# Kernel tuning notes

Hardware: AMD Instinct MI355X
Metric: run time of the kernel (lower is better)

The kernel has to match this reference:

```python
import jax, jax.numpy as jnp
import numpy as np

B, S = 8, 2048
CLIP, H, BN, NC = 512, 512, 256, 10
LN_EPS = 1e-5


def _ln(x, g, b):
    mu = x.mean(-1, keepdims=True)
    var = ((x - mu) ** 2).mean(-1, keepdims=True)
    return (x - mu) * jax.lax.rsqrt(var + LN_EPS) * g + b


def setup_inputs() -> dict:
    key = jax.random.key(0)
    ks = jax.random.split(key, 16)
    sc = lambda i, shp: jax.random.normal(ks[i], shp, jnp.float32) * 0.02
    inp = {
        "local_feat": jax.random.normal(ks[0], (B, S, CLIP), jnp.float32),
        "coords": jax.random.uniform(ks[1], (B, S, 3), jnp.float32),
        "mask": jax.random.randint(ks[2], (B, S), 0, 2) > 0,
        # node encoder
        "w_enc": sc(3, (CLIP, H)), "b_enc": jnp.zeros((H,), jnp.float32),
        "ln1_g": jnp.ones((H,), jnp.float32), "ln1_b": jnp.zeros((H,), jnp.float32),
        # attention projections
        "wq": sc(4, (H, H)), "bq": jnp.zeros((H,), jnp.float32),
        "wk": sc(5, (H, H)), "bk": jnp.zeros((H,), jnp.float32),
        "wv": sc(6, (H, H)), "bv": jnp.zeros((H,), jnp.float32),
        # bottleneck
        "w_bn": sc(7, (H, BN)), "b_bn": jnp.zeros((BN,), jnp.float32),
        "ln2_g": jnp.ones((BN,), jnp.float32), "ln2_b": jnp.zeros((BN,), jnp.float32),
        # classifier
        "w_c1": sc(8, (BN, BN // 2)), "b_c1": jnp.zeros((BN // 2,), jnp.float32),
        "w_c2": sc(9, (BN // 2, NC)), "b_c2": jnp.zeros((NC,), jnp.float32),
    }
    return inp


def reference(local_feat, coords, mask, w_enc, b_enc, ln1_g, ln1_b,
              wq, bq, wk, bk, wv, bv, w_bn, b_bn, ln2_g, ln2_b,
              w_c1, b_c1, w_c2, b_c2):
    # node encoder (dropout is identity in eval)
    h = jax.nn.relu(_ln(local_feat @ w_enc + b_enc, ln1_g, ln1_b))  # [B,S,H]

    # pairwise euclidean distance on (x,y), exp-modulated adjacency
    pos = coords[:, :, :2]
    diff = pos[:, :, None, :] - pos[:, None, :, :]              # [B,S,S,2]
    sq = jnp.sum(diff * diff, axis=-1)                          # [B,S,S]
    dist = jnp.sqrt(jnp.where(sq > 0, sq, 1.0))
    dist = jnp.where(sq > 0, dist, 0.0)
    spatial_adj = jnp.exp(-dist * 5.0)

    q = h @ wq + bq
    k = h @ wk + bk
    v = h @ wv + bv
    scores = jnp.einsum("bsd,btd->bst", q, k) / jnp.sqrt(jnp.float32(H))
    attn = jax.nn.softmax(scores, axis=-1) * spatial_adj        # [B,S,S]
    attn = jnp.where(mask[:, None, :], 0.0, attn)               # zero padded keys

    h_graph = jnp.einsum("bst,btd->bsd", attn, v)               # [B,S,H]
    out = jax.nn.relu(_ln(h_graph @ w_bn + b_bn, ln2_g, ln2_b)) # [B,S,BN]

    valid = (~mask)[:, :, None].astype(out.dtype)               # [B,S,1]
    pooled = (out * valid).sum(1) / jnp.clip(valid.sum(1), 1e-9, None)

    logits = jax.nn.relu(pooled @ w_c1 + b_c1) @ w_c2 + b_c2    # [B,NC]
    return logits, pooled
```

## Files before the change

### kernel.cpp

```cpp
#include <hip/hip_runtime.h>
#include <hip/hip_bf16.h>
#include <stdint.h>


typedef __hip_bfloat16 bf16_t;
typedef __attribute__((ext_vector_type(8))) short bf16x8;
typedef __attribute__((ext_vector_type(4))) float f32x4;

__device__ __forceinline__ void cp16_to_lds(const void* g, void* lds) {
  __builtin_amdgcn_global_load_lds(
      (__attribute__((address_space(1))) void*)(g),
      (__attribute__((address_space(3))) void*)(lds), 16, 0, 0);
}

__device__ __forceinline__ uint pk2(float a, float b) {
  bf16_t x = __float2bfloat16(a), y = __float2bfloat16(b);
  return ((uint)(*(ushort*)&y) << 16) | (*(ushort*)&x);
}
__device__ __forceinline__ float bflo(uint u) { return __uint_as_float(u << 16); }
__device__ __forceinline__ float bfhi(uint u) { return __uint_as_float(u & 0xffff0000u); }

__global__ __launch_bounds__(256) void gemm_bt(
    const bf16_t* __restrict__ A, const bf16_t* __restrict__ B,
    void* __restrict__ Cv, const float* __restrict__ bias, int biasStride,
    float scale, int K, long sA, long sB, long sC, int ldC, int mode)
{
  __shared__ __align__(16) char smem[32768];
  bf16_t* lA = (bf16_t*)smem;
  bf16_t* lB = (bf16_t*)(smem + 16384);
  const int z = blockIdx.z;
  A += (long)z * sA;
  B += (long)z * sB;
  const float* bz = bias ? bias + (long)z * biasStride : nullptr;
  const int m0 = blockIdx.y * 128, n0 = blockIdx.x * 128;
  const int tid = threadIdx.x;
  const int w = tid >> 6, lane = tid & 63;
  const int wm = w >> 1, wn = w & 1;

  const int rr = tid >> 2;
  const int cc = (((tid & 3) ^ ((tid >> 3) & 3)) * 8);
  const bf16_t* a0 = A + (long)(m0 + rr) * K + cc;
  const bf16_t* b0 = B + (long)(n0 + rr) * K + cc;
  const long rowskip = (long)64 * K;

  char* lAc = (char*)lA;
  char* lBc = (char*)lB;
  const int ofs0 = w * 1024;
  const int ofs1 = 4096 + w * 1024;

  f32x4 acc[4][4] = {};
  const int nkt = K >> 6;
  const int quad = lane >> 4;
  const int rsel = lane & 15;
  const int swz = (rsel >> 1) & 3;
  const int kchunkA = (quad ^ swz) * 8;

  for (int kt = 0; kt < nkt; ++kt) {
    __syncthreads();
    cp16_to_lds(a0,                 lAc + ofs0);
    cp16_to_lds(a0 + rowskip,       lAc + ofs1);
    cp16_to_lds(a0 + 32,            lAc + 8192 + ofs0);
    cp16_to_lds(a0 + 32 + rowskip,  lAc + 8192 + ofs1);
    cp16_to_lds(b0,                 lBc + ofs0);
    cp16_to_lds(b0 + rowskip,       lBc + ofs1);
    cp16_to_lds(b0 + 32,            lBc + 8192 + ofs0);
    cp16_to_lds(b0 + 32 + rowskip,  lBc + 8192 + ofs1);
    a0 += 64; b0 += 64;
    __syncthreads();

#pragma unroll
    for (int p = 0; p < 2; ++p) {
      const int pb = p * 4096;
      bf16x8 af[4], bfr[4];
#pragma unroll
      for (int i = 0; i < 4; ++i) {
        af[i]  = *(const bf16x8*)&lA[pb + (wm * 64 + i * 16 + rsel) * 32 + kchunkA];
        bfr[i] = *(const bf16x8*)&lB[pb + (wn * 64 + i * 16 + rsel) * 32 + kchunkA];
      }
#pragma unroll
      for (int i = 0; i < 4; ++i)
#pragma unroll
        for (int j = 0; j < 4; ++j)
          acc[i][j] = __builtin_amdgcn_mfma_f32_16x16x32_bf16(af[i], bfr[j], acc[i][j], 0, 0, 0);
    }
  }

  const int col = lane & 15;
  float bv4[4];
#pragma unroll
  for (int j = 0; j < 4; ++j) {
    const int ng = n0 + wn * 64 + j * 16 + col;
    bv4[j] = bz ? bz[ng] : 0.0f;
  }

  if (mode == 0) {
    char* stb = smem + w * 2176;
    const int nc0 = n0 + wn * 64;
#pragma unroll
    for (int i = 0; i < 4; ++i) {
      __syncthreads();
      bf16_t* st = (bf16_t*)stb;
#pragma unroll
      for (int j = 0; j < 4; ++j)
#pragma unroll
        for (int r = 0; r < 4; ++r)
          st[(quad * 4 + r) * 68 + j * 16 + col] =
              __float2bfloat16(acc[i][j][r] * scale + bv4[j]);
      __syncthreads();
      const int row16 = lane >> 2, cseg = lane & 3;
      const long mrow = m0 + wm * 64 + i * 16 + row16;
      bf16_t* cp = (bf16_t*)Cv + (long)z * sC + mrow * ldC + nc0 + cseg * 16;
      const char* sp = stb + row16 * 136 + cseg * 32;
#pragma unroll
      for (int hh = 0; hh < 2; ++hh) {
        uint2 aa = *(const uint2*)(sp + hh * 16);
        uint2 bb = *(const uint2*)(sp + hh * 16 + 8);
        uint4 vv; vv.x = aa.x; vv.y = aa.y; vv.z = bb.x; vv.w = bb.y;
        *(uint4*)(cp + hh * 8) = vv;
      }
    }
  } else {
#pragma unroll
    for (int j = 0; j < 4; ++j) {
      const int ng = n0 + wn * 64 + j * 16 + col;
#pragma unroll
      for (int i = 0; i < 4; ++i) {
        const int mg = m0 + wm * 64 + i * 16 + quad * 4;
#pragma unroll
        for (int r = 0; r < 4; ++r)
          ((float*)Cv)[(long)z * sC + (long)(mg + r) * ldC + ng] =
              acc[i][j][r] * scale + bv4[j];
      }
    }
  }
}

__global__ __launch_bounds__(256) void weight_prep(
    const float* __restrict__ w0, const float* __restrict__ w1,
    const float* __restrict__ w2, const float* __restrict__ w3,
    const float* __restrict__ w4,
    const float* __restrict__ bq, const float* __restrict__ bk,
    const float* __restrict__ bv,
    bf16_t* __restrict__ outT, float* __restrict__ bias_cat)
{
  const int z = blockIdx.z;
  const int N = (z == 4) ? 256 : 512;
  if (z == 4 && blockIdx.y >= 4) return;
  const float* in = (z == 0) ? w0 : (z == 1) ? w1 : (z == 2) ? w2 : (z == 3) ? w3 : w4;
  bf16_t* out = outT + (long)z * 262144;
  const int k0 = blockIdx.x * 64, n0 = blockIdx.y * 64;
  __shared__ bf16_t tile[64 * 66];
  const int tid = threadIdx.x;
  const int r = tid >> 2, c4 = tid & 3;
  const float* src = in + (long)(k0 + r) * N + n0 + c4 * 16;
  uint* dst = (uint*)&tile[r * 66 + c4 * 16];
  float4 f0 = ((const float4*)src)[0], f1 = ((const float4*)src)[1];
  float4 f2 = ((const float4*)src)[2], f3 = ((const float4*)src)[3];
  dst[0] = pk2(f0.x, f0.y); dst[1] = pk2(f0.z, f0.w);
  dst[2] = pk2(f1.x, f1.y); dst[3] = pk2(f1.z, f1.w);
  dst[4] = pk2(f2.x, f2.y); dst[5] = pk2(f2.z, f2.w);
  dst[6] = pk2(f3.x, f3.y); dst[7] = pk2(f3.z, f3.w);
  __syncthreads();
  bf16_t* og = out + (long)(n0 + r) * 512 + k0 + c4 * 16;
  uint ov[8];
#pragma unroll
  for (int j = 0; j < 16; j += 2) {
    const ushort lo = *(const ushort*)&tile[(c4 * 16 + j) * 66 + r];
    const ushort hi = *(const ushort*)&tile[(c4 * 16 + j + 1) * 66 + r];
    ov[j >> 1] = ((uint)hi << 16) | lo;
  }
  uint4 o0, o1;
  o0.x = ov[0]; o0.y = ov[1]; o0.z = ov[2]; o0.w = ov[3];
  o1.x = ov[4]; o1.y = ov[5]; o1.z = ov[6]; o1.w = ov[7];
  ((uint4*)og)[0] = o0;
  ((uint4*)og)[1] = o1;
  if (z >= 1 && z <= 3 && blockIdx.x == 0 && blockIdx.y == 0) {
    const float* bs = (z == 1) ? bq : (z == 2) ? bk : bv;
    bias_cat[(z - 1) * 512 + tid] = bs[tid];
    bias_cat[(z - 1) * 512 + 256 + tid] = bs[256 + tid];
  }
}

__global__ __launch_bounds__(256) void transpose_bf16_k(
    const bf16_t* __restrict__ in, bf16_t* __restrict__ o)
{
  __shared__ bf16_t tile[64 * 66];
  const int b = blockIdx.z, t0 = blockIdx.x * 64, d0 = blockIdx.y * 64;
  const int tid = threadIdx.x;
  const int r = tid >> 2, c4 = tid & 3;
  const uint4* src = (const uint4*)(in + ((long)b * 2048 + t0 + r) * 512 + d0 + c4 * 16);
  uint* dst = (uint*)&tile[r * 66 + c4 * 16];
  uint4 g0 = src[0], g1 = src[1];
  dst[0] = g0.x; dst[1] = g0.y; dst[2] = g0.z; dst[3] = g0.w;
  dst[4] = g1.x; dst[5] = g1.y; dst[6] = g1.z; dst[7] = g1.w;
  __syncthreads();
  bf16_t* dstg = o + ((long)b * 512 + d0 + r) * 2048 + t0 + c4 * 16;
  uint ov[8];
#pragma unroll
  for (int k = 0; k < 16; k += 2) {
    const ushort lo = *(const ushort*)&tile[(c4 * 16 + k) * 66 + r];
    const ushort hi = *(const ushort*)&tile[(c4 * 16 + k + 1) * 66 + r];
    ov[k >> 1] = ((uint)hi << 16) | lo;
  }
  uint4 o0, o1;
  o0.x = ov[0]; o0.y = ov[1]; o0.z = ov[2]; o0.w = ov[3];
  o1.x = ov[4]; o1.y = ov[5]; o1.z = ov[6]; o1.w = ov[7];
  ((uint4*)dstg)[0] = o0;
  ((uint4*)dstg)[1] = o1;
}

__global__ __launch_bounds__(256) void cast_bf16_v(
    const float4* __restrict__ in, uint2* __restrict__ o, int n4) {
  const int i = blockIdx.x * 256 + threadIdx.x;
  if (i < n4) {
    const float4 f = in[i];
    uint2 r; r.x = pk2(f.x, f.y); r.y = pk2(f.z, f.w);
    o[i] = r;
  }
}

__global__ __launch_bounds__(256) void ln_relu_h(
    bf16_t* __restrict__ X, const float* __restrict__ g, const float* __restrict__ b)
{
  const int tid = threadIdx.x;
  const int lane = tid & 63, w = tid >> 6;
  const long row = (long)blockIdx.x * 4 + w;
  bf16_t* xp = X + row * 512 + lane * 8;
  const uint4 pkv = *(const uint4*)xp;
  const uint va[4] = {pkv.x, pkv.y, pkv.z, pkv.w};
  float v[8];
  float s = 0.0f, q = 0.0f;
#pragma unroll
  for (int i = 0; i < 4; ++i) {
    v[2 * i] = bflo(va[i]); v[2 * i + 1] = bfhi(va[i]);
    s += v[2 * i] + v[2 * i + 1];
    q += v[2 * i] * v[2 * i] + v[2 * i + 1] * v[2 * i + 1];
  }
  for (int o = 32; o; o >>= 1) { s += __shfl_down(s, o); q += __shfl_down(q, o); }
  s = __shfl(s, 0); q = __shfl(q, 0);
  const float mu = s * (1.0f / 512.0f);
  const float rs = rsqrtf(q * (1.0f / 512.0f) - mu * mu + 1e-5f);
  const float4 g0 = ((const float4*)(g + lane * 8))[0], g1 = ((const float4*)(g + lane * 8))[1];
  const float4 b0 = ((const float4*)(b + lane * 8))[0], b1 = ((const float4*)(b + lane * 8))[1];
  const float gg[8] = {g0.x, g0.y, g0.z, g0.w, g1.x, g1.y, g1.z, g1.w};
  const float bb[8] = {b0.x, b0.y, b0.z, b0.w, b1.x, b1.y, b1.z, b1.w};
  uint ov[4];
#pragma unroll
  for (int i = 0; i < 4; ++i) {
    const float y0 = fmaxf((v[2 * i] - mu) * rs * gg[2 * i] + bb[2 * i], 0.0f);
    const float y1 = fmaxf((v[2 * i + 1] - mu) * rs * gg[2 * i + 1] + bb[2 * i + 1], 0.0f);
    ov[i] = pk2(y0, y1);
  }
  uint4 st; st.x = ov[0]; st.y = ov[1]; st.z = ov[2]; st.w = ov[3];
  *(uint4*)xp = st;
}

__global__ __launch_bounds__(256) void softmax_adj(
    bf16_t* __restrict__ SC, const float* __restrict__ coords,
    const int* __restrict__ mask)
{
  const int bs = blockIdx.x;
  const int b = bs >> 11, s = bs & 2047;
  const long base = (long)bs * 2048;
  const int tid = threadIdx.x;
  const uint4 pkv = *(const uint4*)(SC + base + tid * 8);
  const uint va[4] = {pkv.x, pkv.y, pkv.z, pkv.w};
  float rv[8];
  float mx = -3.0e38f;
#pragma unroll
  for (int i = 0; i < 4; ++i) {
    rv[2 * i] = bflo(va[i]); rv[2 * i + 1] = bfhi(va[i]);
    mx = fmaxf(mx, fmaxf(rv[2 * i], rv[2 * i + 1]));
  }
  for (int o = 32; o; o >>= 1) mx = fmaxf(mx, __shfl_down(mx, o));
  __shared__ float sm[8];
  const int w = tid >> 6, lane = tid & 63;
  if (!lane) sm[w] = mx;
  __syncthreads();
  mx = fmaxf(fmaxf(sm[0], sm[1]), fmaxf(sm[2], sm[3]));
  float sum = 0.0f;
#pragma unroll
  for (int i = 0; i < 8; ++i) { rv[i] = __expf(rv[i] - mx); sum += rv[i]; }
  for (int o = 32; o; o >>= 1) sum += __shfl_down(sum, o);
  if (!lane) sm[4 + w] = sum;
  __syncthreads();
  const float inv = 1.0f / (sm[4] + sm[5] + sm[6] + sm[7]);
  const float px = coords[((long)b * 2048 + s) * 3];
  const float py = coords[((long)b * 2048 + s) * 3 + 1];
  const int t0 = tid * 8;
  const float* cb = coords + ((long)b * 2048 + t0) * 3;
  const int* mb = mask + b * 2048 + t0;
  uint ov[4];
#pragma unroll
  for (int i = 0; i < 8; ++i) {
    const float dx = px - cb[i * 3], dy = py - cb[i * 3 + 1];
    const float adj = __expf(-5.0f * sqrtf(dx * dx + dy * dy));
    const float val = mb[i] ? 0.0f : rv[i] * inv * adj;
    bf16_t bt = __float2bfloat16(val);
    const ushort u = *(const ushort*)&bt;
    if (i & 1) ov[i >> 1] |= ((uint)u << 16);
    else       ov[i >> 1] = u;
  }
  uint4 st; st.x = ov[0]; st.y = ov[1]; st.z = ov[2]; st.w = ov[3];
  *(uint4*)(SC + base + t0) = st;
}

__global__ __launch_bounds__(256) void ln2_pool(
    const float* __restrict__ X, const float* __restrict__ g, const float* __restrict__ bt,
    const int* __restrict__ mask, float* __restrict__ pacc)
{
  const int tid = threadIdx.x;
  const int row0 = blockIdx.x * 16;
  const int w = tid >> 6, lane = tid & 63;
  __shared__ float sm[8];
  const float gv = g[tid], bv = bt[tid];
  float acc = 0.0f;
  for (int r = 0; r < 16; ++r) {
    const int row = row0 + r;
    const float x = X[(long)row * 256 + tid];
    float s = x, q = x * x;
    for (int o = 32; o; o >>= 1) { s += __shfl_down(s, o); q += __shfl_down(q, o); }
    if (!lane) { sm[w] = s; sm[4 + w] = q; }
    __syncthreads();
    const float S = sm[0] + sm[1] + sm[2] + sm[3];
    const float Q = sm[4] + sm[5] + sm[6] + sm[7];
    const float mu = S * (1.0f / 256.0f);
    const float rs = rsqrtf(Q * (1.0f / 256.0f) - mu * mu + 1e-5f);
    const float y = fmaxf((x - mu) * rs * gv + bv, 0.0f);
    if (!mask[row]) acc += y;
    __syncthreads();
  }
  atomicAdd(&pacc[(row0 >> 11) * 256 + tid], acc);
}

__global__ __launch_bounds__(256) void classifier_k(
    const float* __restrict__ pacc, const int* __restrict__ mask,
    const float* __restrict__ w1, const float* __restrict__ b1,
    const float* __restrict__ w2, const float* __restrict__ b2,
    float* __restrict__ out)
{
  const int tid = threadIdx.x;
  __shared__ float pooled[2048];
  __shared__ float hidden[1024];
  __shared__ float cnt[8];
  if (tid < 8) cnt[tid] = 0.0f;
  __syncthreads();
  {
    const int* mb = mask + tid * 64;
    int c = 0;
#pragma unroll 8
    for (int i = 0; i < 64; ++i) c += mb[i] ? 0 : 1;
    atomicAdd(&cnt[tid >> 5], (float)c);
  }
  __syncthreads();
  for (int i = tid; i < 2048; i += 256) {
    const float p = pacc[i] / fmaxf(cnt[i >> 8], 1e-9f);
    pooled[i] = p;
    out[80 + i] = p;
  }
  __syncthreads();
  for (int o = tid; o < 1024; o += 256) {
    const int bb = o >> 7, j = o & 127;
    float s = b1[j];
    const float* pb = pooled + bb * 256;
    for (int c = 0; c < 256; ++c) s += pb[c] * w1[c * 128 + j];
    hidden[o] = fmaxf(s, 0.0f);
  }
  __syncthreads();
  if (tid < 80) {
    const int bb = tid / 10, j = tid - bb * 10;
    float s = b2[j];
    const float* hb = hidden + bb * 128;
    for (int c = 0; c < 128; ++c) s += hb[c] * w2[c * 10 + j];
    out[tid] = s;
  }
}

extern "C" void kernel_launch(void* const* d_in, const int* in_sizes, int n_in,
                              void* d_out, int out_size, void* d_ws, size_t ws_size,
                              hipStream_t stream)
{
  const float* lf   = (const float*)d_in[0];
  const float* co   = (const float*)d_in[1];
  const int*   mk   = (const int*)d_in[2];
  const float* wenc = (const float*)d_in[3];
  const float* benc = (const float*)d_in[4];
  const float* g1   = (const float*)d_in[5];
  const float* be1  = (const float*)d_in[6];
  const float* wq   = (const float*)d_in[7];
  const float* bq   = (const float*)d_in[8];
  const float* wk   = (const float*)d_in[9];
  const float* bk   = (const float*)d_in[10];
  const float* wv   = (const float*)d_in[11];
  const float* bvp  = (const float*)d_in[12];
  const float* wbn  = (const float*)d_in[13];
  const float* bbn  = (const float*)d_in[14];
  const float* g2   = (const float*)d_in[15];
  const float* be2  = (const float*)d_in[16];
  const float* w1   = (const float*)d_in[17];
  const float* b1   = (const float*)d_in[18];
  const float* w2   = (const float*)d_in[19];
  const float* b2   = (const float*)d_in[20];
  float* out = (float*)d_out;
  char* ws = (char*)d_ws;

  bf16_t* featb = (bf16_t*)(ws + 0);
  bf16_t* wT    = (bf16_t*)(ws + 16777216);
  bf16_t* wencT = wT;
  bf16_t* wqT   = wT + 262144;
  bf16_t* wbnT  = wT + 4 * 262144;
  float*  bias_cat = (float*)(ws + 19398656);
  bf16_t* h     = (bf16_t*)(ws + 19404800);
  bf16_t* qkv   = (bf16_t*)(ws + 36182016);
  bf16_t* vT    = (bf16_t*)(ws + 86513664);
  bf16_t* sc    = (bf16_t*)(ws + 103290880);
  bf16_t* hg    = (bf16_t*)(ws + 0);
  float*  bnp   = (float*)(ws + 36182016);
  float*  pacc  = (float*)(ws + 52959232);

  if (ws_size < 170399744) return;

  cast_bf16_v<<<8192, 256, 0, stream>>>((const float4*)lf, (uint2*)featb, 2097152);
  weight_prep<<<dim3(8, 8, 5), 256, 0, stream>>>(wenc, wq, wk, wv, wbn, bq, bk, bvp,
                                                 wT, bias_cat);

  gemm_bt<<<dim3(4, 128, 1), 256, 0, stream>>>(featb, wencT, h, benc, 0, 1.0f, 512,
                                               0, 0, 0, 512, 0);
  ln_relu_h<<<4096, 256, 0, stream>>>(h, g1, be1);
  gemm_bt<<<dim3(4, 128, 3), 256, 0, stream>>>(h, wqT, qkv, bias_cat, 512, 1.0f, 512,
                                               0, 262144, 8388608, 512, 0);
  transpose_bf16_k<<<dim3(32, 8, 8), 256, 0, stream>>>(qkv + 16777216, vT);
  gemm_bt<<<dim3(16, 16, 8), 256, 0, stream>>>(qkv, qkv + 8388608, sc, nullptr, 0,
                                               0.044194173824159216f, 512,
                                               1048576, 1048576, 4194304, 2048, 0);
  softmax_adj<<<16384, 256, 0, stream>>>(sc, co, mk);
  gemm_bt<<<dim3(4, 16, 8), 256, 0, stream>>>(sc, vT, hg, nullptr, 0, 1.0f, 2048,
                                              4194304, 1048576, 1048576, 512, 0);
  gemm_bt<<<dim3(2, 128, 1), 256, 0, stream>>>(hg, wbnT, bnp, bbn, 0, 1.0f, 512,
                                               0, 0, 0, 256, 2);
  hipMemsetAsync(pacc, 0, 8192, stream);
  ln2_pool<<<1024, 256, 0, stream>>>(bnp, g2, be2, mk, pacc);
  classifier_k<<<1, 256, 0, stream>>>(pacc, mk, w1, b1, w2, b2, out);
}
```

Baseline: 405.7 us.

## Double-buffer GEMM K-panels to overlap global-to-LDS loads with MFMA

Restructures the gemm_bt main loop into 32-wide K panels held in two LDS buffers. The next panel is issued with global_load_lds while MFMAs run on the current one, so load latency is hidden behind compute rather than exposed between barriers. Barrier count per 64 of K stays the same. The scheme relies on the barrier waiting for the outstanding async LDS loads, and it only speeds up the GEMM parts of the pipeline.

```diff
diff --git a/kernel.cpp b/kernel.cpp
--- a/kernel.cpp
+++ b/kernel.cpp
@@ -49,41 +49,44 @@
   const int ofs1 = 4096 + w * 1024;
 
   f32x4 acc[4][4] = {};
-  const int nkt = K >> 6;
   const int quad = lane >> 4;
   const int rsel = lane & 15;
   const int swz = (rsel >> 1) & 3;
   const int kchunkA = (quad ^ swz) * 8;
 
-  for (int kt = 0; kt < nkt; ++kt) {
+#define STAGE(kofs, bofs) do {                                   \
+    cp16_to_lds(a0 + (kofs),           lAc + (bofs) + ofs0);     \
+    cp16_to_lds(a0 + (kofs) + rowskip, lAc + (bofs) + ofs1);     \
+    cp16_to_lds(b0 + (kofs),           lBc + (bofs) + ofs0);     \
+    cp16_to_lds(b0 + (kofs) + rowskip, lBc + (bofs) + ofs1);     \
+  } while (0)
+
+#define COMPUTE(pbase) do {                                                        \
+    bf16x8 af[4], bfr[4];                                                          \
+    _Pragma("unroll")                                                              \
+    for (int i = 0; i < 4; ++i) {                                                  \
+      af[i]  = *(const bf16x8*)&lA[(pbase) + (wm * 64 + i * 16 + rsel) * 32 + kchunkA]; \
+      bfr[i] = *(const bf16x8*)&lB[(pbase) + (wn * 64 + i * 16 + rsel) * 32 + kchunkA]; \
+    }                                                                              \
+    _Pragma("unroll")                                                              \
+    for (int i = 0; i < 4; ++i)                                                    \
+      _Pragma("unroll")                                                            \
+      for (int j = 0; j < 4; ++j)                                                  \
+        acc[i][j] = __builtin_amdgcn_mfma_f32_16x16x32_bf16(af[i], bfr[j], acc[i][j], 0, 0, 0); \
+  } while (0)
+
+  const int npan = K >> 5;
+  STAGE(0, 0);
+  for (int pp = 0; pp < npan; pp += 2) {
     __syncthreads();
-    cp16_to_lds(a0,                 lAc + ofs0);
-    cp16_to_lds(a0 + rowskip,       lAc + ofs1);
-    cp16_to_lds(a0 + 32,            lAc + 8192 + ofs0);
-    cp16_to_lds(a0 + 32 + rowskip,  lAc + 8192 + ofs1);
-    cp16_to_lds(b0,                 lBc + ofs0);
-    cp16_to_lds(b0 + rowskip,       lBc + ofs1);
-    cp16_to_lds(b0 + 32,            lBc + 8192 + ofs0);
-    cp16_to_lds(b0 + 32 + rowskip,  lBc + 8192 + ofs1);
-    a0 += 64; b0 += 64;
+    STAGE((pp + 1) * 32, 8192);
+    COMPUTE(0);
     __syncthreads();
-
-#pragma unroll
-    for (int p = 0; p < 2; ++p) {
-      const int pb = p * 4096;
-      bf16x8 af[4], bfr[4];
-#pragma unroll
-      for (int i = 0; i < 4; ++i) {
-        af[i]  = *(const bf16x8*)&lA[pb + (wm * 64 + i * 16 + rsel) * 32 + kchunkA];
-        bfr[i] = *(const bf16x8*)&lB[pb + (wn * 64 + i * 16 + rsel) * 32 + kchunkA];
-      }
-#pragma unroll
-      for (int i = 0; i < 4; ++i)
-#pragma unroll
-        for (int j = 0; j < 4; ++j)
-          acc[i][j] = __builtin_amdgcn_mfma_f32_16x16x32_bf16(af[i], bfr[j], acc[i][j], 0, 0, 0);
-    }
-  }
+    if (pp + 2 < npan) STAGE((pp + 2) * 32, 0);
+    COMPUTE(4096);
+  }
+#undef STAGE
+#undef COMPUTE
 
   const int col = lane & 15;
   float bv4[4];
```

Result: slower. 414.7 us (+2.2%).

## Emit Q/K as fp8 and V transposed from QKV GEMM; fp8 score GEMM

Applied to the files above, without the earlier changes.

The QKV projection becomes a dedicated kernel that writes Q and K as fp8 bytes and writes V directly in transposed bf16 layout, so the separate transpose kernel is no longer needed. The score GEMM now reads fp8 Q/K and uses fp8 MFMA instructions, which halves its operand bytes and doubles the k-depth per load. This lowers memory traffic and removes one launch. The cost is reduced precision in the attention scores, which could hurt accuracy.

```diff
diff --git a/kernel.cpp b/kernel.cpp
--- a/kernel.cpp
+++ b/kernel.cpp
@@ -4,6 +4,7 @@
 
 
 typedef __hip_bfloat16 bf16_t;
+typedef unsigned char u8;
 typedef __attribute__((ext_vector_type(8))) short bf16x8;
 typedef __attribute__((ext_vector_type(4))) float f32x4;
 
@@ -131,6 +132,218 @@
           ((float*)Cv)[(long)z * sC + (long)(mg + r) * ldC + ng] =
               acc[i][j][r] * scale + bv4[j];
       }
+    }
+  }
+}
+
+__global__ __launch_bounds__(256) void gemm_qkv(
+    const bf16_t* __restrict__ A, const bf16_t* __restrict__ wT,
+    const float* __restrict__ bias_cat, u8* __restrict__ o8,
+    bf16_t* __restrict__ vT)
+{
+  __shared__ __align__(16) char smem[32768];
+  bf16_t* lA = (bf16_t*)smem;
+  bf16_t* lB = (bf16_t*)(smem + 16384);
+  const int z = blockIdx.z;
+  const bf16_t* B = wT + (long)(z + 1) * 262144;
+  const float* bz = bias_cat + (long)z * 512;
+  const int K = 512;
+  const int m0 = blockIdx.y * 128, n0 = blockIdx.x * 128;
+  const int tid = threadIdx.x;
+  const int w = tid >> 6, lane = tid & 63;
+  const int wm = w >> 1, wn = w & 1;
+
+  const int rr = tid >> 2;
+  const int cc = (((tid & 3) ^ ((tid >> 3) & 3)) * 8);
+  const bf16_t* a0 = A + (long)(m0 + rr) * K + cc;
+  const bf16_t* b0 = B + (long)(n0 + rr) * K + cc;
+  const long rowskip = (long)64 * K;
+
+  char* lAc = (char*)lA;
+  char* lBc = (char*)lB;
+  const int ofs0 = w * 1024;
+  const int ofs1 = 4096 + w * 1024;
+
+  f32x4 acc[4][4] = {};
+  const int quad = lane >> 4;
+  const int rsel = lane & 15;
+  const int swz = (rsel >> 1) & 3;
+  const int kchunkA = (quad ^ swz) * 8;
+
+  for (int kt = 0; kt < 8; ++kt) {
+    __syncthreads();
+    cp16_to_lds(a0,                 lAc + ofs0);
+    cp16_to_lds(a0 + rowskip,       lAc + ofs1);
+    cp16_to_lds(a0 + 32,            lAc + 8192 + ofs0);
+    cp16_to_lds(a0 + 32 + rowskip,  lAc + 8192 + ofs1);
+    cp16_to_lds(b0,                 lBc + ofs0);
+    cp16_to_lds(b0 + rowskip,       lBc + ofs1);
+    cp16_to_lds(b0 + 32,            lBc + 8192 + ofs0);
+    cp16_to_lds(b0 + 32 + rowskip,  lBc + 8192 + ofs1);
+    a0 += 64; b0 += 64;
+    __syncthreads();
+
+#pragma unroll
+    for (int p = 0; p < 2; ++p) {
+      const int pb = p * 4096;
+      bf16x8 af[4], bfr[4];
+#pragma unroll
+      for (int i = 0; i < 4; ++i) {
+        af[i]  = *(const bf16x8*)&lA[pb + (wm * 64 + i * 16 + rsel) * 32 + kchunkA];
+        bfr[i] = *(const bf16x8*)&lB[pb + (wn * 64 + i * 16 + rsel) * 32 + kchunkA];
+      }
+#pragma unroll
+      for (int i = 0; i < 4; ++i)
+#pragma unroll
+        for (int j = 0; j < 4; ++j)
+          acc[i][j] = __builtin_amdgcn_mfma_f32_16x16x32_bf16(af[i], bfr[j], acc[i][j], 0, 0, 0);
+    }
+  }
+
+  const int col = lane & 15;
+  float bv4[4];
+#pragma unroll
+  for (int j = 0; j < 4; ++j) bv4[j] = bz[n0 + wn * 64 + j * 16 + col];
+  const int nc0 = n0 + wn * 64;
+
+  if (z < 2) {
+    u8* stb = (u8*)(smem + w * 2176);
+    u8* O = o8 + (long)z * 8388608;
+#pragma unroll
+    for (int i = 0; i < 4; ++i) {
+      __syncthreads();
+#pragma unroll
+      for (int j = 0; j < 4; ++j) {
+        uint pk = 0;
+        pk = __builtin_amdgcn_cvt_pk_fp8_f32(acc[i][j][0] + bv4[j],
+                                             acc[i][j][1] + bv4[j], pk, false);
+        pk = __builtin_amdgcn_cvt_pk_fp8_f32(acc[i][j][2] + bv4[j],
+                                             acc[i][j][3] + bv4[j], pk, true);
+        stb[(quad * 4 + 0) * 72 + j * 16 + col] = (u8)(pk);
+        stb[(quad * 4 + 1) * 72 + j * 16 + col] = (u8)(pk >> 8);
+        stb[(quad * 4 + 2) * 72 + j * 16 + col] = (u8)(pk >> 16);
+        stb[(quad * 4 + 3) * 72 + j * 16 + col] = (u8)(pk >> 24);
+      }
+      __syncthreads();
+      const int trow = lane >> 2, seg = lane & 3;
+      const long mrow = m0 + wm * 64 + i * 16 + trow;
+      *(uint4*)(O + mrow * 512 + nc0 + seg * 16) =
+          *(const uint4*)(stb + trow * 72 + seg * 16);
+    }
+  } else {
+    bf16_t* st = (bf16_t*)(smem + w * 2176);
+    const int bt = blockIdx.y >> 4;
+    const int t0g = (m0 & 2047) + wm * 64;
+#pragma unroll
+    for (int j = 0; j < 4; ++j) {
+      __syncthreads();
+#pragma unroll
+      for (int i = 0; i < 4; ++i) {
+        uint2 v2;
+        v2.x = pk2(acc[i][j][0] + bv4[j], acc[i][j][1] + bv4[j]);
+        v2.y = pk2(acc[i][j][2] + bv4[j], acc[i][j][3] + bv4[j]);
+        *(uint2*)&st[col * 68 + i * 16 + quad * 4] = v2;
+      }
+      __syncthreads();
+      const int drow = lane >> 2, seg = lane & 3;
+      const int d = nc0 + j * 16 + drow;
+      bf16_t* dst = vT + ((long)(bt * 512 + d)) * 2048 + t0g;
+#pragma unroll
+      for (int rd = 0; rd < 2; ++rd)
+        *(uint4*)(dst + rd * 32 + seg * 8) =
+            *(const uint4*)((const char*)st + drow * 136 + rd * 64 + seg * 16);
+    }
+  }
+}
+
+__global__ __launch_bounds__(256) void gemm_sc_fp8(
+    const u8* __restrict__ A, const u8* __restrict__ B,
+    bf16_t* __restrict__ C, float scale)
+{
+  __shared__ __align__(16) char smem[32768];
+  const int K = 512;
+  const int z = blockIdx.z;
+  A += (long)z * 1048576;
+  B += (long)z * 1048576;
+  const int m0 = blockIdx.y * 128, n0 = blockIdx.x * 128;
+  const int tid = threadIdx.x;
+  const int w = tid >> 6, lane = tid & 63;
+  const int wm = w >> 1, wn = w & 1;
+
+  const int rr = tid >> 2;
+  const int ccB = (((tid & 3) ^ ((tid >> 3) & 3)) * 16);
+  const u8* a0 = A + (long)(m0 + rr) * K + ccB;
+  const u8* b0 = B + (long)(n0 + rr) * K + ccB;
+  const long rowskip = (long)64 * K;
+
+  char* lAc = smem;
+  char* lBc = smem + 16384;
+  const int ofs0 = w * 1024;
+  const int ofs1 = 4096 + w * 1024;
+
+  f32x4 acc[4][4] = {};
+  const int quad = lane >> 4;
+  const int rsel = lane & 15;
+  const int swz = (rsel >> 1) & 3;
+
+  for (int kt = 0; kt < 4; ++kt) {
+    __syncthreads();
+    cp16_to_lds(a0,                  lAc + ofs0);
+    cp16_to_lds(a0 + rowskip,        lAc + ofs1);
+    cp16_to_lds(a0 + 64,             lAc + 8192 + ofs0);
+    cp16_to_lds(a0 + 64 + rowskip,   lAc + 8192 + ofs1);
+    cp16_to_lds(b0,                  lBc + ofs0);
+    cp16_to_lds(b0 + rowskip,        lBc + ofs1);
+    cp16_to_lds(b0 + 64,             lBc + 8192 + ofs0);
+    cp16_to_lds(b0 + 64 + rowskip,   lBc + 8192 + ofs1);
+    a0 += 128; b0 += 128;
+    __syncthreads();
+
+#pragma unroll
+    for (int p = 0; p < 2; ++p) {
+      const int pb = p * 8192;
+#pragma unroll
+      for (int ks = 0; ks < 2; ++ks) {
+        const int gr = ((ks * 2 + (quad >> 1)) ^ swz) * 16 + (quad & 1) * 8;
+        long av[4], bv[4];
+#pragma unroll
+        for (int i = 0; i < 4; ++i) {
+          av[i] = *(const long*)(lAc + pb + (wm * 64 + i * 16 + rsel) * 64 + gr);
+          bv[i] = *(const long*)(lBc + pb + (wn * 64 + i * 16 + rsel) * 64 + gr);
+        }
+#pragma unroll
+        for (int i = 0; i < 4; ++i)
+#pragma unroll
+          for (int j = 0; j < 4; ++j)
+            acc[i][j] = __builtin_amdgcn_mfma_f32_16x16x32_fp8_fp8(av[i], bv[j], acc[i][j], 0, 0, 0);
+      }
+    }
+  }
+
+  const int col = lane & 15;
+  char* stb = smem + w * 2176;
+  const int nc0 = n0 + wn * 64;
+#pragma unroll
+  for (int i = 0; i < 4; ++i) {
+    __syncthreads();
+    bf16_t* st = (bf16_t*)stb;
+#pragma unroll
+    for (int j = 0; j < 4; ++j)
+#pragma unroll
+      for (int r = 0; r < 4; ++r)
+        st[(quad * 4 + r) * 68 + j * 16 + col] =
+            __float2bfloat16(acc[i][j][r] * scale);
+    __syncthreads();
+    const int row16 = lane >> 2, cseg = lane & 3;
+    const long mrow = m0 + wm * 64 + i * 16 + row16;
+    bf16_t* cp = C + (long)z * 4194304 + mrow * 2048 + nc0 + cseg * 16;
+    const char* sp = stb + row16 * 136 + cseg * 32;
+#pragma unroll
+    for (int hh = 0; hh < 2; ++hh) {
+      uint2 aa = *(const uint2*)(sp + hh * 16);
+      uint2 bb = *(const uint2*)(sp + hh * 16 + 8);
+      uint4 vv; vv.x = aa.x; vv.y = aa.y; vv.z = bb.x; vv.w = bb.y;
+      *(uint4*)(cp + hh * 8) = vv;
     }
   }
 }
@@ -179,34 +392,6 @@
     bias_cat[(z - 1) * 512 + tid] = bs[tid];
     bias_cat[(z - 1) * 512 + 256 + tid] = bs[256 + tid];
   }
-}
-
-__global__ __launch_bounds__(256) void transpose_bf16_k(
-    const bf16_t* __restrict__ in, bf16_t* __restrict__ o)
-{
-  __shared__ bf16_t tile[64 * 66];
-  const int b = blockIdx.z, t0 = blockIdx.x * 64, d0 = blockIdx.y * 64;
-  const int tid = threadIdx.x;
-  const int r = tid >> 2, c4 = tid & 3;
-  const uint4* src = (const uint4*)(in + ((long)b * 2048 + t0 + r) * 512 + d0 + c4 * 16);
-  uint* dst = (uint*)&tile[r * 66 + c4 * 16];
-  uint4 g0 = src[0], g1 = src[1];
-  dst[0] = g0.x; dst[1] = g0.y; dst[2] = g0.z; dst[3] = g0.w;
-  dst[4] = g1.x; dst[5] = g1.y; dst[6] = g1.z; dst[7] = g1.w;
-  __syncthreads();
-  bf16_t* dstg = o + ((long)b * 512 + d0 + r) * 2048 + t0 + c4 * 16;
-  uint ov[8];
-#pragma unroll
-  for (int k = 0; k < 16; k += 2) {
-    const ushort lo = *(const ushort*)&tile[(c4 * 16 + k) * 66 + r];
-    const ushort hi = *(const ushort*)&tile[(c4 * 16 + k + 1) * 66 + r];
-    ov[k >> 1] = ((uint)hi << 16) | lo;
-  }
-  uint4 o0, o1;
-  o0.x = ov[0]; o0.y = ov[1]; o0.z = ov[2]; o0.w = ov[3];
-  o1.x = ov[4]; o1.y = ov[5]; o1.z = ov[6]; o1.w = ov[7];
-  ((uint4*)dstg)[0] = o0;
-  ((uint4*)dstg)[1] = o1;
 }
 
 __global__ __launch_bounds__(256) void cast_bf16_v(
@@ -407,18 +592,17 @@
   bf16_t* featb = (bf16_t*)(ws + 0);
   bf16_t* wT    = (bf16_t*)(ws + 16777216);
   bf16_t* wencT = wT;
-  bf16_t* wqT   = wT + 262144;
   bf16_t* wbnT  = wT + 4 * 262144;
   float*  bias_cat = (float*)(ws + 19398656);
   bf16_t* h     = (bf16_t*)(ws + 19404800);
-  bf16_t* qkv   = (bf16_t*)(ws + 36182016);
-  bf16_t* vT    = (bf16_t*)(ws + 86513664);
-  bf16_t* sc    = (bf16_t*)(ws + 103290880);
+  u8*     q8    = (u8*)(ws + 36182016);
+  bf16_t* vT    = (bf16_t*)(ws + 52959232);
+  bf16_t* sc    = (bf16_t*)(ws + 69736448);
   bf16_t* hg    = (bf16_t*)(ws + 0);
   float*  bnp   = (float*)(ws + 36182016);
   float*  pacc  = (float*)(ws + 52959232);
 
-  if (ws_size < 170399744) return;
+  if (ws_size < 136845312) return;
 
   cast_bf16_v<<<8192, 256, 0, stream>>>((const float4*)lf, (uint2*)featb, 2097152);
   weight_prep<<<dim3(8, 8, 5), 256, 0, stream>>>(wenc, wq, wk, wv, wbn, bq, bk, bvp,
@@ -427,12 +611,9 @@
   gemm_bt<<<dim3(4, 128, 1), 256, 0, stream>>>(featb, wencT, h, benc, 0, 1.0f, 512,
                                                0, 0, 0, 512, 0);
   ln_relu_h<<<4096, 256, 0, stream>>>(h, g1, be1);
-  gemm_bt<<<dim3(4, 128, 3), 256, 0, stream>>>(h, wqT, qkv, bias_cat, 512, 1.0f, 512,
-                                               0, 262144, 8388608, 512, 0);
-  transpose_bf16_k<<<dim3(32, 8, 8), 256, 0, stream>>>(qkv + 16777216, vT);
-  gemm_bt<<<dim3(16, 16, 8), 256, 0, stream>>>(qkv, qkv + 8388608, sc, nullptr, 0,
-                                               0.044194173824159216f, 512,
-                                               1048576, 1048576, 4194304, 2048, 0);
+  gemm_qkv<<<dim3(4, 128, 3), 256, 0, stream>>>(h, wT, bias_cat, q8, vT);
+  gemm_sc_fp8<<<dim3(16, 16, 8), 256, 0, stream>>>(q8, q8 + 8388608, sc,
+                                                   0.044194173824159216f);
   softmax_adj<<<16384, 256, 0, stream>>>(sc, co, mk);
   gemm_bt<<<dim3(4, 16, 8), 256, 0, stream>>>(sc, vT, hg, nullptr, 0, 1.0f, 2048,
                                               4194304, 1048576, 1048576, 512, 0);
```

After: 365.3 us. -9.9%, faster.
